# Performance work log

Hardware: AMD Instinct MI355X
Metric: run time of the kernel (lower is better)

## Reference

```python
import jax, jax.numpy as jnp
import numpy as np

# q_config constants
W_IN, E_IN = 8, 4          # data_in_width, data_in_exponent_width
R_W = 6                     # data_r_width
W_OUT, E_OUT = 8, 4        # data_out_width, data_out_exponent_width (= data_n_width)
EXP_SUM_UF = 4              # exp_sum_underflow_bits
DIV_UF = 4                  # division_underflow_bits
W_DATA, E_DATA = 8, 4      # data_width, data_exponent_width

N, D = 8192, 2048


def integer_quantizer(x, width, frac_width):
    s = 2.0 ** frac_width
    lo, hi = -(2.0 ** (width - 1)), 2.0 ** (width - 1) - 1
    return jnp.clip(jnp.round(x * s), lo, hi) / s


def integer_floor_quantizer(x, width, frac_width):
    s = 2.0 ** frac_width
    lo, hi = -(2.0 ** (width - 1)), 2.0 ** (width - 1) - 1
    return jnp.clip(jnp.floor(x * s), lo, hi) / s


def mxint_quant(x, width, exponent_width):
    # MXInt block quantization with parallelism [1,1]: per-element shared exponent.
    e_hi, e_lo = 2.0 ** (exponent_width - 1) - 1, -(2.0 ** (exponent_width - 1))
    ax = jnp.abs(x)
    e = jnp.ceil(jnp.log2(jnp.where(ax == 0, 1.0, ax)))
    e = jnp.clip(e, e_lo, e_hi)
    scale = 2.0 ** (width - 1)
    m = jnp.clip(jnp.round(x * 2.0 ** (-e) * scale), -scale, scale - 1)
    qx = m * 2.0 ** e / scale
    return qx, m, e


def setup_inputs() -> dict:
    key = jax.random.key(0)
    x = jax.random.normal(key, (N, D), dtype=jnp.float32)
    return {"x": x}


def reference(x):
    # ---- MXIntHardwareExp: quantize input, range-reduce x = r + n*ln2 ----
    qx, _, _ = mxint_quant(x, W_IN, E_IN)
    log2e, _, _ = mxint_quant(jnp.float32(np.log2(np.e)), 8, 4)
    y = qx * log2e
    y = integer_floor_quantizer(y, E_OUT + R_W - 1, R_W - 1)
    n = jnp.floor(y)
    r = y - n                                # r in [0, 1)
    mexp = integer_quantizer(2.0 ** r, W_OUT, W_OUT - 2) * 2.0 ** (W_OUT - 2)
    eexp = n                                 # qexp = mexp * 2^eexp / 2^(W_OUT-2)

    # ---- exp_sum: exponent-aligned integer accumulation over dim 1 ----
    ms = (mexp * 2.0 ** EXP_SUM_UF).T        # [D, N]
    es = eexp.T                              # [D, N]

    def step(carry, me):
        out, emax = carry
        mi, ei = me
        new_emax = jnp.maximum(emax, ei)
        out = jnp.floor(out * 2.0 ** (emax - new_emax)) + jnp.floor(mi * 2.0 ** (ei - new_emax))
        return (out, new_emax), None

    (mexp_sum, eexp_sum), _ = jax.lax.scan(step, (ms[0], es[0]), (ms[1:], es[1:]))
    # mexp_sum, eexp_sum: [N]

    # ---- division: per-element mantissa integer division by the sum ----
    mout = jnp.floor(mexp * 2.0 ** (DIV_UF + EXP_SUM_UF) / mexp_sum[:, None])
    eout = eexp - eexp_sum[:, None]
    qout = mout * 2.0 ** eout / 2.0 ** DIV_UF
    qout, _, _ = mxint_quant(qout, W_DATA, E_DATA)
    return qout
```

## Files before the change

kernel.cpp:

```cpp
#include <hip/hip_runtime.h>


#define D_DIM 2048
#define TPB   256

__device__ __forceinline__ unsigned bmax4(unsigned x, unsigned y) {
    const unsigned d     = (x | 0x80808080u) - y;
    const unsigned flags = d & 0x80808080u;
    const unsigned mask  = (flags - (flags >> 7)) | flags;
    return (x & mask) | (y & ~mask);
}

__global__ __launch_bounds__(TPB, 6) void mxint_softmax_kernel(const float* __restrict__ x,
                                                               float* __restrict__ out) {
    const int t    = threadIdx.x;
    const int lane = t & 63;
    const int wid  = t >> 6;
    const int half = wid & 1;
    const int r    = wid >> 1;
    const int row  = blockIdx.x * 2 + r;

    __shared__ unsigned short     s_pk[512];
    __shared__ float              s_fin[2][512];
    __shared__ int                s_rmax[4];
    __shared__ unsigned long long s_part[4];

    const size_t base = (size_t)row * D_DIM + half * 1024 + lane * 4;
    float4 v[4];
#pragma unroll
    for (int i = 0; i < 4; ++i)
        v[i] = *(const float4*)(x + base + i * 256);

#pragma unroll
    for (int q = 0; q < 2; ++q) {
        const int idx = t + 256 * q;
        const float a = fmaf((float)(idx & 31), 0.03125f, 6.0f);
        const int  me = (int)rintf(__builtin_amdgcn_exp2f(a));
        s_pk[idx] = (unsigned short)(me << 4);
    }

    int yq[16];
    unsigned pe = 0;
#pragma unroll
    for (int i = 0; i < 4; ++i) {
        const float xs4[4] = {v[i].x, v[i].y, v[i].z, v[i].w};
        int rmaxr = -256;
#pragma unroll
        for (int k = 0; k < 4; ++k) {
            const unsigned b  = __float_as_uint(xs4[k]) & 0x7fffffffu;
            const unsigned tb = b + 0x7fffffu;
            const unsigned tc = min(max(tb, 0x3B800000u), 0x43000000u);
            const unsigned es = tc & 0xFF800000u;
            const float    su  = __uint_as_float(0x82800000u - es);
            const float    fac = __uint_as_float(es + 0xFF380000u);
            const float    mi  = __builtin_amdgcn_fmed3f(rintf(xs4[k] * su), -128.0f, 127.0f);
            int y = (int)floorf(mi * fac);
            y = min(255, max(-256, y));
            yq[4 * i + k] = y;
            rmaxr = max(rmaxr, y);
        }
        pe |= (unsigned)((rmaxr >> 5) + 8) << (8 * i);
    }

    unsigned s = pe;
#pragma unroll
    for (int d = 1; d < 64; d <<= 1) {
        const unsigned o = __shfl_up(s, d, 64);
        if (lane >= d) s = bmax4(s, o);
    }
    unsigned ex = __shfl_up(s, 1, 64);
    if (lane == 0) ex = 0;
    const unsigned bc = __shfl(s, 63, 64);
    const int wtot = max(max((int)(bc & 255u), (int)((bc >> 8) & 255u)),
                         max((int)((bc >> 16) & 255u), (int)(bc >> 24)));
    s_rmax[wid] = wtot;
    __syncthreads();

    const int c0 = half ? s_rmax[wid - 1] : 0;

    unsigned partial = 0;
    int crun = c0;
#pragma unroll
    for (int i = 0; i < 4; ++i) {
        const int sx   = (int)((ex >> (8 * i)) & 255u);
        int a = max(crun, sx);
#pragma unroll
        for (int k = 0; k < 4; ++k) {
            const int y  = yq[4 * i + k];
            const int h  = (y >> 5) + 8;
            a = max(a, h);
            const unsigned me4 = s_pk[y + 256];
            partial += (me4 >> (a - h)) << a;
        }
        crun = max(crun, (int)((bc >> (8 * i)) & 255u));
    }

    const unsigned ps = partial + __shfl_xor(partial, 1, 64);
    unsigned long long p64 = ps;
#pragma unroll
    for (int d = 2; d < 64; d <<= 1) p64 += __shfl_xor(p64, d, 64);
    s_part[wid] = p64;
    __syncthreads();

    const unsigned long long tot = s_part[2 * r] + s_part[2 * r + 1];
    const int      Estar8 = max(s_rmax[2 * r], s_rmax[2 * r + 1]);
    const unsigned msum   = (unsigned)(tot >> Estar8);
    const unsigned magic  = (unsigned)(274877906944.0 / (double)msum) + 1u;

    const int tr = t & 127;
#pragma unroll
    for (int q = 0; q < 4; ++q) {
        const int      idx  = tr + 128 * q;
        const unsigned me4  = s_pk[idx];
        const unsigned mout = __umulhi(me4 << 4, magic) >> 6;
        const int      e8   = idx >> 5;
        const int      eoutn = Estar8 - e8;
        const int      bl   = 32 - __clz((int)(mout | 1u));
        const int      pw2  = ((mout & (mout - 1u)) == 0u) ? 1 : 0;
        const int      clog = bl - pw2;
        const int      sq   = min(7 - clog, 11 - eoutn);
        const int      rs   = 8 - sq;
        const unsigned u    = mout << 8;
        const unsigned bse  = u >> rs;
        const unsigned frac = u & ((1u << rs) - 1u);
        const unsigned hlf  = 1u << (rs - 1);
        unsigned m2 = bse + (((frac > hlf) || (frac == hlf && (bse & 1u))) ? 1u : 0u);
        m2 = min(m2, 127u);
        const int ef = max(clog - eoutn - 4, -8);
        s_fin[r][idx] = (float)m2 * __uint_as_float((unsigned)(ef + 120) << 23);
    }
    __syncthreads();

    float* orow = out + base;
#pragma unroll
    for (int i = 0; i < 4; ++i) {
        float r4[4];
#pragma unroll
        for (int k = 0; k < 4; ++k)
            r4[k] = s_fin[r][yq[4 * i + k] + 256];
        const float4 o4 = {r4[0], r4[1], r4[2], r4[3]};
        *(float4*)(orow + i * 256) = o4;
    }
}

extern "C" void kernel_launch(void* const* d_in, const int* in_sizes, int n_in,
                              void* d_out, int out_size, void* d_ws, size_t ws_size,
                              hipStream_t stream) {
    const float* x = (const float*)d_in[0];
    float*       o = (float*)d_out;
    const int rows = in_sizes[0] / D_DIM;
    mxint_softmax_kernel<<<rows / 2, TPB, 0, stream>>>(x, o);
}
```

Baseline: 109.9 us.

## Process one row per block with four waves instead of two rows per block

Each 256-thread block now handles a single row, with each of the four waves covering interleaved 1024-element halves. The exponent prefix-max carry is rebuilt from all four waves' packed per-chunk maxima. Per-thread register and loop work is halved and the grid doubles, which is meant to raise occupancy and latency hiding on a memory-bound kernel (launch bounds raised to 8). In exchange, each block repeats the LUT setup and division-table pass for only one row, and the block-level reductions become slightly more complex.

```diff
diff --git a/kernel.cpp b/kernel.cpp
--- a/kernel.cpp
+++ b/kernel.cpp
@@ -11,25 +11,23 @@
     return (x & mask) | (y & ~mask);
 }
 
-__global__ __launch_bounds__(TPB, 6) void mxint_softmax_kernel(const float* __restrict__ x,
+__global__ __launch_bounds__(TPB, 8) void mxint_softmax_kernel(const float* __restrict__ x,
                                                                float* __restrict__ out) {
     const int t    = threadIdx.x;
     const int lane = t & 63;
     const int wid  = t >> 6;
-    const int half = wid & 1;
-    const int r    = wid >> 1;
-    const int row  = blockIdx.x * 2 + r;
+    const int row  = blockIdx.x;
 
     __shared__ unsigned short     s_pk[512];
-    __shared__ float              s_fin[2][512];
-    __shared__ int                s_rmax[4];
+    __shared__ float              s_fin[512];
+    __shared__ unsigned           s_rmax[4];
     __shared__ unsigned long long s_part[4];
 
-    const size_t base = (size_t)row * D_DIM + half * 1024 + lane * 4;
-    float4 v[4];
+    const size_t base = (size_t)row * D_DIM + t * 4;
+    float4 v[2];
 #pragma unroll
-    for (int i = 0; i < 4; ++i)
-        v[i] = *(const float4*)(x + base + i * 256);
+    for (int i = 0; i < 2; ++i)
+        v[i] = *(const float4*)(x + base + i * 1024);
 
 #pragma unroll
     for (int q = 0; q < 2; ++q) {
@@ -39,10 +37,10 @@
         s_pk[idx] = (unsigned short)(me << 4);
     }
 
-    int yq[16];
+    int yq[8];
     unsigned pe = 0;
 #pragma unroll
-    for (int i = 0; i < 4; ++i) {
+    for (int i = 0; i < 2; ++i) {
         const float xs4[4] = {v[i].x, v[i].y, v[i].z, v[i].w};
         int rmaxr = -256;
 #pragma unroll
@@ -71,19 +69,24 @@
     unsigned ex = __shfl_up(s, 1, 64);
     if (lane == 0) ex = 0;
     const unsigned bc = __shfl(s, 63, 64);
-    const int wtot = max(max((int)(bc & 255u), (int)((bc >> 8) & 255u)),
-                         max((int)((bc >> 16) & 255u), (int)(bc >> 24)));
-    s_rmax[wid] = wtot;
+    s_rmax[wid] = bc;
     __syncthreads();
 
-    const int c0 = half ? s_rmax[wid - 1] : 0;
+    const unsigned w0 = s_rmax[0], w1 = s_rmax[1], w2 = s_rmax[2], w3 = s_rmax[3];
+    int c0 = 0, c1p = 0;
+    if (wid > 0) { c0 = (int)(w0 & 255u);          c1p = (int)((w0 >> 8) & 255u); }
+    if (wid > 1) { c0 = max(c0, (int)(w1 & 255u)); c1p = max(c1p, (int)((w1 >> 8) & 255u)); }
+    if (wid > 2) { c0 = max(c0, (int)(w2 & 255u)); c1p = max(c1p, (int)((w2 >> 8) & 255u)); }
+    const unsigned mall = bmax4(bmax4(w0, w1), bmax4(w2, w3));
+    const int A0     = (int)(mall & 255u);
+    const int c1     = max(A0, c1p);
+    const int Estar8 = max(A0, (int)((mall >> 8) & 255u));
 
     unsigned partial = 0;
-    int crun = c0;
+    const int cs[2] = {c0, c1};
 #pragma unroll
-    for (int i = 0; i < 4; ++i) {
-        const int sx   = (int)((ex >> (8 * i)) & 255u);
-        int a = max(crun, sx);
+    for (int i = 0; i < 2; ++i) {
+        int a = max(cs[i], (int)((ex >> (8 * i)) & 255u));
 #pragma unroll
         for (int k = 0; k < 4; ++k) {
             const int y  = yq[4 * i + k];
@@ -92,7 +95,6 @@
             const unsigned me4 = s_pk[y + 256];
             partial += (me4 >> (a - h)) << a;
         }
-        crun = max(crun, (int)((bc >> (8 * i)) & 255u));
     }
 
     const unsigned ps = partial + __shfl_xor(partial, 1, 64);
@@ -102,15 +104,13 @@
     s_part[wid] = p64;
     __syncthreads();
 
-    const unsigned long long tot = s_part[2 * r] + s_part[2 * r + 1];
-    const int      Estar8 = max(s_rmax[2 * r], s_rmax[2 * r + 1]);
+    const unsigned long long tot = s_part[0] + s_part[1] + s_part[2] + s_part[3];
     const unsigned msum   = (unsigned)(tot >> Estar8);
     const unsigned magic  = (unsigned)(274877906944.0 / (double)msum) + 1u;
 
-    const int tr = t & 127;
 #pragma unroll
-    for (int q = 0; q < 4; ++q) {
-        const int      idx  = tr + 128 * q;
+    for (int q = 0; q < 2; ++q) {
+        const int      idx  = t + 256 * q;
         const unsigned me4  = s_pk[idx];
         const unsigned mout = __umulhi(me4 << 4, magic) >> 6;
         const int      e8   = idx >> 5;
@@ -127,19 +127,19 @@
         unsigned m2 = bse + (((frac > hlf) || (frac == hlf && (bse & 1u))) ? 1u : 0u);
         m2 = min(m2, 127u);
         const int ef = max(clog - eoutn - 4, -8);
-        s_fin[r][idx] = (float)m2 * __uint_as_float((unsigned)(ef + 120) << 23);
+        s_fin[idx] = (float)m2 * __uint_as_float((unsigned)(ef + 120) << 23);
     }
     __syncthreads();
 
     float* orow = out + base;
 #pragma unroll
-    for (int i = 0; i < 4; ++i) {
+    for (int i = 0; i < 2; ++i) {
         float r4[4];
 #pragma unroll
         for (int k = 0; k < 4; ++k)
-            r4[k] = s_fin[r][yq[4 * i + k] + 256];
+            r4[k] = s_fin[yq[4 * i + k] + 256];
         const float4 o4 = {r4[0], r4[1], r4[2], r4[3]};
-        *(float4*)(orow + i * 256) = o4;
+        *(float4*)(orow + i * 1024) = o4;
     }
 }
 
@@ -149,5 +149,5 @@
     const float* x = (const float*)d_in[0];
     float*       o = (float*)d_out;
     const int rows = in_sizes[0] / D_DIM;
-    mxint_softmax_kernel<<<rows / 2, TPB, 0, stream>>>(x, o);
+    mxint_softmax_kernel<<<rows, TPB, 0, stream>>>(x, o);
 }
```

After: 111.7 us. About the same (+1.7%).

## Replicate LDS lookup tables to cut bank conflicts and use nontemporal global I/O

Applied to the files above, without the earlier changes.

Duplicates the mantissa and final-value lookup tables in shared memory into two padded copies, with odd and even lanes reading different copies so random gathers hit fewer bank conflicts. It also switches the streaming input loads and output stores to nontemporal builtins so they bypass cache retention. The cost is more LDS use, which could limit occupancy, and duplicated table writes.

```diff
diff --git a/kernel.cpp b/kernel.cpp
--- a/kernel.cpp
+++ b/kernel.cpp
@@ -3,6 +3,8 @@
 
 #define D_DIM 2048
 #define TPB   256
+
+typedef float vf4 __attribute__((ext_vector_type(4)));
 
 __device__ __forceinline__ unsigned bmax4(unsigned x, unsigned y) {
     const unsigned d     = (x | 0x80808080u) - y;
@@ -20,23 +22,25 @@
     const int r    = wid >> 1;
     const int row  = blockIdx.x * 2 + r;
 
-    __shared__ unsigned short     s_pk[512];
-    __shared__ float              s_fin[2][512];
+    __shared__ unsigned short     s_pk[2][528];
+    __shared__ float              s_fin[2][2][520];
     __shared__ int                s_rmax[4];
     __shared__ unsigned long long s_part[4];
 
     const size_t base = (size_t)row * D_DIM + half * 1024 + lane * 4;
-    float4 v[4];
+    vf4 v[4];
 #pragma unroll
     for (int i = 0; i < 4; ++i)
-        v[i] = *(const float4*)(x + base + i * 256);
+        v[i] = __builtin_nontemporal_load((const vf4*)(x + base + i * 256));
 
 #pragma unroll
     for (int q = 0; q < 2; ++q) {
         const int idx = t + 256 * q;
         const float a = fmaf((float)(idx & 31), 0.03125f, 6.0f);
         const int  me = (int)rintf(__builtin_amdgcn_exp2f(a));
-        s_pk[idx] = (unsigned short)(me << 4);
+        const unsigned short pv = (unsigned short)(me << 4);
+        s_pk[0][idx] = pv;
+        s_pk[1][idx] = pv;
     }
 
     int yq[16];
@@ -78,6 +82,7 @@
 
     const int c0 = half ? s_rmax[wid - 1] : 0;
 
+    const unsigned short* pk = s_pk[lane & 1];
     unsigned partial = 0;
     int crun = c0;
 #pragma unroll
@@ -89,7 +94,7 @@
             const int y  = yq[4 * i + k];
             const int h  = (y >> 5) + 8;
             a = max(a, h);
-            const unsigned me4 = s_pk[y + 256];
+            const unsigned me4 = pk[y + 256];
             partial += (me4 >> (a - h)) << a;
         }
         crun = max(crun, (int)((bc >> (8 * i)) & 255u));
@@ -111,7 +116,7 @@
 #pragma unroll
     for (int q = 0; q < 4; ++q) {
         const int      idx  = tr + 128 * q;
-        const unsigned me4  = s_pk[idx];
+        const unsigned me4  = s_pk[0][idx];
         const unsigned mout = __umulhi(me4 << 4, magic) >> 6;
         const int      e8   = idx >> 5;
         const int      eoutn = Estar8 - e8;
@@ -127,19 +132,21 @@
         unsigned m2 = bse + (((frac > hlf) || (frac == hlf && (bse & 1u))) ? 1u : 0u);
         m2 = min(m2, 127u);
         const int ef = max(clog - eoutn - 4, -8);
-        s_fin[r][idx] = (float)m2 * __uint_as_float((unsigned)(ef + 120) << 23);
+        const float fv = (float)m2 * __uint_as_float((unsigned)(ef + 120) << 23);
+        s_fin[r][0][idx] = fv;
+        s_fin[r][1][idx] = fv;
     }
     __syncthreads();
 
+    const float* tab = s_fin[r][lane & 1];
     float* orow = out + base;
 #pragma unroll
     for (int i = 0; i < 4; ++i) {
-        float r4[4];
+        vf4 o4;
 #pragma unroll
         for (int k = 0; k < 4; ++k)
-            r4[k] = s_fin[r][yq[4 * i + k] + 256];
-        const float4 o4 = {r4[0], r4[1], r4[2], r4[3]};
-        *(float4*)(orow + i * 256) = o4;
+            o4[k] = tab[yq[4 * i + k] + 256];
+        __builtin_nontemporal_store(o4, (vf4*)(orow + i * 256));
     }
 }
 
```

Result: slower. 116.4 us (+5.9%).
